# Performance work log

Measured on AMD Instinct MI355X. Metric: run time of the kernel, lower is better.

The kernel has to match this reference:

```python
import jax, jax.numpy as jnp
import numpy as np

B, T, D, H = 8, 2048, 1024, 64

def setup_inputs() -> dict:
    key = jax.random.key(0)
    kx, kq, kk, kv = jax.random.split(key, 4)
    x = jax.random.normal(kx, (B, T, D), dtype=jnp.float32)
    # Linear(embd_size, head_size, bias=False) weights, stored as [D, H] for x @ W
    Wq = jax.random.normal(kq, (D, H), dtype=jnp.float32) * (D ** -0.5)
    Wk = jax.random.normal(kk, (D, H), dtype=jnp.float32) * (D ** -0.5)
    Wv = jax.random.normal(kv, (D, H), dtype=jnp.float32) * (D ** -0.5)
    return {"x": x, "Wq": Wq, "Wk": Wk, "Wv": Wv}

def reference(x, Wq, Wk, Wv):
    Tcur = x.shape[1]
    q = x @ Wq  # [B, T, H]
    k = x @ Wk
    v = x @ Wv
    scores = jnp.einsum('bth,bsh->bts', q, k)
    # NOTE: faithful to source quirk: scores are MULTIPLIED by sqrt(T)
    scores = scores * (Tcur ** 0.5)
    causal = jnp.tril(jnp.ones((Tcur, Tcur), dtype=bool))
    scores = jnp.where(causal, scores, -jnp.inf)
    attn = jax.nn.softmax(scores, axis=2)  # dropout p=0.0 -> identity
    return jnp.einsum('bts,bsh->bth', attn, v)
```

## Files before the change

### kernel.cpp

```cpp
#include <hip/hip_runtime.h>
#include <hip/hip_bf16.h>

#define BB 8
#define TT 2048
#define DD 1024
#define HH 64
#define NROWS (BB*TT)
#define SCALE 45.25483399593904f
#define SPLIT 4

typedef __attribute__((ext_vector_type(8))) short short8;
typedef __attribute__((ext_vector_type(4))) float f32x4;

__device__ inline ushort bf16rne(float f) {
    unsigned u = __float_as_uint(f);
    return (ushort)((u + 0x7fffu + ((u >> 16) & 1u)) >> 16);
}
__device__ inline void bfsplit(float f, ushort& hi, ushort& lo) {
    hi = bf16rne(f);
    float fh = __uint_as_float(((unsigned)hi) << 16);
    lo = bf16rne(f - fh);
}
__device__ inline void split_pack8(const float* v, int4& h4, int4& l4) {
    ushort h[8], l[8];
    #pragma unroll
    for (int j = 0; j < 8; ++j) bfsplit(v[j], h[j], l[j]);
    h4 = make_int4((int)(h[0] | ((unsigned)h[1] << 16)), (int)(h[2] | ((unsigned)h[3] << 16)),
                   (int)(h[4] | ((unsigned)h[5] << 16)), (int)(h[6] | ((unsigned)h[7] << 16)));
    l4 = make_int4((int)(l[0] | ((unsigned)l[1] << 16)), (int)(l[2] | ((unsigned)l[3] << 16)),
                   (int)(l[4] | ((unsigned)l[5] << 16)), (int)(l[6] | ((unsigned)l[7] << 16)));
}

__device__ inline void gload_lds16(const void* g, void* l) {
    __builtin_amdgcn_global_load_lds(
        (const __attribute__((address_space(1))) unsigned int*)(uintptr_t)(g),
        (__attribute__((address_space(3))) unsigned int*)(uintptr_t)(l),
        16, 0, 0);
}

__global__ __launch_bounds__(256) void wprep_kernel(
        const float* __restrict__ Wq, const float* __restrict__ Wk,
        const float* __restrict__ Wv,
        ushort* __restrict__ WpHi, ushort* __restrict__ WpLo) {
    __shared__ float ws[64 * 65];
    const int m = blockIdx.x >> 4;
    const int c = blockIdx.x & 15;
    const float* W = (m == 0) ? Wq : (m == 1) ? Wk : Wv;
    const int tid = threadIdx.x;

    #pragma unroll
    for (int p = 0; p < 4; ++p) {
        int i = tid + p * 256;
        int r = i >> 4, q4 = i & 15;
        float4 v = *(const float4*)(W + (size_t)(c * 64 + r) * 64 + q4 * 4);
        ws[r * 65 + q4 * 4 + 0] = v.x;
        ws[r * 65 + q4 * 4 + 1] = v.y;
        ws[r * 65 + q4 * 4 + 2] = v.z;
        ws[r * 65 + q4 * 4 + 3] = v.w;
    }
    __syncthreads();

    #pragma unroll
    for (int p = 0; p < 2; ++p) {
        int gi = tid + p * 256;
        int nn = gi >> 3, g8 = gi & 7;
        int o  = g8 ^ (nn & 7);
        float v[8];
        #pragma unroll
        for (int j = 0; j < 8; ++j) v[j] = ws[(o * 8 + j) * 65 + nn];
        int4 h4, l4; split_pack8(v, h4, l4);
        size_t base = (size_t)c * 12288 + (size_t)(m * 64 + nn) * 64 + g8 * 8;
        *(int4*)(WpHi + base) = h4;
        *(int4*)(WpLo + base) = l4;
    }
}

__global__ __launch_bounds__(256) void qkv_kernel(
        const float* __restrict__ x,
        const ushort* __restrict__ WpHi, const ushort* __restrict__ WpLo,
        float* __restrict__ Qo, ushort* __restrict__ KhiP,
        ushort* __restrict__ KloP, ushort* __restrict__ VtP) {
    __shared__ ushort Ahi[32 * 64], Alo[32 * 64];
    __shared__ ushort Bhi[192 * 64], Blo[192 * 64];
    const int tid  = threadIdx.x;
    const int lane = tid & 63;
    const int w    = tid >> 6;
    const int n15  = lane & 15;
    const int g    = lane >> 4;
    const int csw  = n15 & 7;
    const int row0 = blockIdx.x * 32;

    f32x4 acc[2][3];
    #pragma unroll
    for (int ms = 0; ms < 2; ++ms)
        #pragma unroll
        for (int nt = 0; nt < 3; ++nt) acc[ms][nt] = (f32x4)0.f;

    const int ar = tid >> 3, aoc = tid & 7;
    const float* xrow = x + (size_t)(row0 + ar) * 1024 + aoc * 8;
    const int adi = ar * 64 + ((aoc ^ (ar & 7)) << 3);

    for (int c = 0; c < 16; ++c) {
        __syncthreads();
        {
            const ushort* sh = WpHi + (size_t)c * 12288 + (size_t)lane * 8;
            const ushort* sl = WpLo + (size_t)c * 12288 + (size_t)lane * 8;
            #pragma unroll
            for (int p = 0; p < 6; ++p) {
                int j = w * 6 + p;
                gload_lds16(sh + j * 512, &Bhi[j * 512]);
                gload_lds16(sl + j * 512, &Blo[j * 512]);
            }
        }
        {
            const float* src = xrow + c * 64;
            float v[8];
            *(float4*)v       = *(const float4*)src;
            *(float4*)(v + 4) = *(const float4*)(src + 4);
            int4 h4, l4; split_pack8(v, h4, l4);
            *(int4*)&Ahi[adi] = h4;
            *(int4*)&Alo[adi] = l4;
        }
        __syncthreads();

        #pragma unroll
        for (int kh = 0; kh < 2; ++kh) {
            short8 afh[2], afl[2], bfh[3], bfl[3];
            #pragma unroll
            for (int ms = 0; ms < 2; ++ms) {
                int ridx = (ms * 16 + n15) * 64 + (((4 * kh + g) ^ csw) << 3);
                afh[ms] = *(const short8*)&Ahi[ridx];
                afl[ms] = *(const short8*)&Alo[ridx];
            }
            #pragma unroll
            for (int nt = 0; nt < 3; ++nt) {
                int nr = w * 48 + nt * 16 + n15;
                int ridx = nr * 64 + (((4 * kh + g) ^ csw) << 3);
                bfh[nt] = *(const short8*)&Bhi[ridx];
                bfl[nt] = *(const short8*)&Blo[ridx];
            }
            #pragma unroll
            for (int nt = 0; nt < 3; ++nt)
                #pragma unroll
                for (int ms = 0; ms < 2; ++ms) {
                    acc[ms][nt] = __builtin_amdgcn_mfma_f32_16x16x32_bf16(
                        afh[ms], bfh[nt], acc[ms][nt], 0, 0, 0);
                    acc[ms][nt] = __builtin_amdgcn_mfma_f32_16x16x32_bf16(
                        afl[ms], bfh[nt], acc[ms][nt], 0, 0, 0);
                    acc[ms][nt] = __builtin_amdgcn_mfma_f32_16x16x32_bf16(
                        afh[ms], bfl[nt], acc[ms][nt], 0, 0, 0);
                }
        }
    }

    const int b  = row0 >> 11;
    const int t0 = row0 & 2047;
    #pragma unroll
    for (int nt = 0; nt < 3; ++nt) {
        const int nglob = w * 48 + nt * 16 + n15;
        const int mat = nglob >> 6;
        const int h = nglob & 63;
        #pragma unroll
        for (int ms = 0; ms < 2; ++ms) {
            const int mb = row0 + ms * 16 + 4 * g;
            if (mat == 0) {
                #pragma unroll
                for (int r = 0; r < 4; ++r)
                    Qo[(size_t)(mb + r) * 64 + h] = acc[ms][nt][r];
            } else if (mat == 1) {
                #pragma unroll
                for (int r = 0; r < 4; ++r) {
                    ushort hi, lo; bfsplit(acc[ms][nt][r], hi, lo);
                    KhiP[(size_t)(mb + r) * 64 + h] = hi;
                    KloP[(size_t)(mb + r) * 64 + h] = lo;
                }
            } else {
                ushort pk[4];
                #pragma unroll
                for (int r = 0; r < 4; ++r) pk[r] = bf16rne(acc[ms][nt][r]);
                const int tloc = t0 + ms * 16 + 4 * g;
                *(uint2*)&VtP[((size_t)(b * 64 + h)) * 2048 + tloc] =
                    make_uint2(pk[0] | ((unsigned)pk[1] << 16),
                               pk[2] | ((unsigned)pk[3] << 16));
            }
        }
    }
}

__global__ __launch_bounds__(128) void attn_kernel(
        const float* __restrict__ Q, const ushort* __restrict__ Khi,
        const ushort* __restrict__ Klo, const ushort* __restrict__ Vt,
        float* __restrict__ Pacc, float* __restrict__ Pm,
        float* __restrict__ Pl) {
    __shared__ ushort KhiL[64 * 64];
    __shared__ ushort KloL[64 * 64];
    __shared__ ushort VtL[64 * 64];
    const int tid  = threadIdx.x;
    const int lane = tid & 63;
    const int w    = tid >> 6;
    const int n    = lane & 15;
    const int g    = lane >> 4;
    const int b    = blockIdx.y;
    const int xx   = blockIdx.x;
    const int qt   = 63 - (xx >> 2);
    const int sp   = xx & 3;
    const int q0   = qt * 32;
    const int qmin = q0 + w * 16;
    const int qrow = qmin + n;
    const int csw  = n & 7;
    const int ntiles = (q0 >> 6) + 1;
    const int it0  = (ntiles * sp) >> 2;
    const int it1  = (ntiles * (sp + 1)) >> 2;

    short8 qhi0, qhi1, qlo0, qlo1;
    {
        const float* qp = Q + ((size_t)b * TT + qrow) * HH + 8 * g;
        float v0[8], v1[8];
        *(float4*)(v0)     = *(const float4*)(qp);
        *(float4*)(v0 + 4) = *(const float4*)(qp + 4);
        *(float4*)(v1)     = *(const float4*)(qp + 32);
        *(float4*)(v1 + 4) = *(const float4*)(qp + 36);
        #pragma unroll
        for (int j = 0; j < 8; ++j) {
            ushort hi, lo;
            bfsplit(v0[j], hi, lo); qhi0[j] = (short)hi; qlo0[j] = (short)lo;
            bfsplit(v1[j], hi, lo); qhi1[j] = (short)hi; qlo1[j] = (short)lo;
        }
    }

    f32x4 accO[4];
    #pragma unroll
    for (int t = 0; t < 4; ++t) accO[t] = (f32x4)0.f;
    float m = -1e30f, l = 0.f;

    const ushort* gkh = Khi + (size_t)b * TT * HH;
    const ushort* gkl = Klo + (size_t)b * TT * HH;
    const ushort* gvt = Vt + (size_t)b * 64 * TT;

    const int crow = lane >> 3;
    const int coct = lane & 7;

    for (int it = it0; it < it1; ++it) {
        const int kb = it * 64;
        __syncthreads();
        #pragma unroll
        for (int p = 0; p < 4; ++p) {
            const int cc  = w * 4 + p;
            const int row = (cc << 3) + crow;
            const int soc = coct ^ (row & 7);
            gload_lds16(gkh + (size_t)(kb + row) * HH + (soc << 3), &KhiL[cc << 9]);
            gload_lds16(gkl + (size_t)(kb + row) * HH + (soc << 3), &KloL[cc << 9]);
            gload_lds16(gvt + (size_t)row * TT + kb + (soc << 3),   &VtL[cc << 9]);
        }
        __syncthreads();

        f32x4 s4[4];
        #pragma unroll
        for (int s = 0; s < 4; ++s) {
            const int keyl = 16 * s + n;
            const ushort* kbase = &KhiL[keyl << 6];
            const ushort* lbase = &KloL[keyl << 6];
            short8 kh0 = *(const short8*)(kbase + ((g ^ csw) << 3));
            short8 kh1 = *(const short8*)(kbase + (((4 + g) ^ csw) << 3));
            short8 kl0 = *(const short8*)(lbase + ((g ^ csw) << 3));
            short8 kl1 = *(const short8*)(lbase + (((4 + g) ^ csw) << 3));
            f32x4 a = (f32x4)0.f;
            a = __builtin_amdgcn_mfma_f32_16x16x32_bf16(kh0, qhi0, a, 0, 0, 0);
            a = __builtin_amdgcn_mfma_f32_16x16x32_bf16(kh1, qhi1, a, 0, 0, 0);
            a = __builtin_amdgcn_mfma_f32_16x16x32_bf16(kl0, qhi0, a, 0, 0, 0);
            a = __builtin_amdgcn_mfma_f32_16x16x32_bf16(kl1, qhi1, a, 0, 0, 0);
            a = __builtin_amdgcn_mfma_f32_16x16x32_bf16(kh0, qlo0, a, 0, 0, 0);
            a = __builtin_amdgcn_mfma_f32_16x16x32_bf16(kh1, qlo1, a, 0, 0, 0);
            s4[s] = a;
        }

        float sm[16];
        if (kb + 63 > qmin) {
            #pragma unroll
            for (int s = 0; s < 4; ++s)
                #pragma unroll
                for (int r = 0; r < 4; ++r) {
                    int keyg = kb + 16 * s + 4 * g + r;
                    sm[s * 4 + r] = (keyg <= qrow) ? s4[s][r] * SCALE : -1e30f;
                }
        } else {
            #pragma unroll
            for (int s = 0; s < 4; ++s)
                #pragma unroll
                for (int r = 0; r < 4; ++r) sm[s * 4 + r] = s4[s][r] * SCALE;
        }
        float pm = sm[0];
        #pragma unroll
        for (int i = 1; i < 16; ++i) pm = fmaxf(pm, sm[i]);
        pm = fmaxf(pm, __shfl_xor(pm, 16));
        pm = fmaxf(pm, __shfl_xor(pm, 32));
        float mn = fmaxf(m, pm);
        float es = __expf(m - mn);
        float p[16], ps = 0.f;
        #pragma unroll
        for (int i = 0; i < 16; ++i) { p[i] = __expf(sm[i] - mn); ps += p[i]; }
        ps += __shfl_xor(ps, 16);
        ps += __shfl_xor(ps, 32);
        l = l * es + ps;
        m = mn;
        #pragma unroll
        for (int t = 0; t < 4; ++t)
            #pragma unroll
            for (int r = 0; r < 4; ++r) accO[t][r] *= es;

        short8 pf0, pf1;
        #pragma unroll
        for (int j = 0; j < 4; ++j) {
            pf0[j]     = (short)bf16rne(p[0 * 4 + j]);
            pf0[j + 4] = (short)bf16rne(p[1 * 4 + j]);
            pf1[j]     = (short)bf16rne(p[2 * 4 + j]);
            pf1[j + 4] = (short)bf16rne(p[3 * 4 + j]);
        }

        #pragma unroll
        for (int t = 0; t < 4; ++t) {
            const int h = 16 * t + n;
            const ushort* vb = &VtL[h << 6];
            union { int2 d[2]; short8 v; } u0, u1;
            u0.d[0] = *(const int2*)(vb + ((4 * g) ^ (csw << 3)));
            u0.d[1] = *(const int2*)(vb + ((16 + 4 * g) ^ (csw << 3)));
            u1.d[0] = *(const int2*)(vb + ((32 + 4 * g) ^ (csw << 3)));
            u1.d[1] = *(const int2*)(vb + ((48 + 4 * g) ^ (csw << 3)));
            accO[t] = __builtin_amdgcn_mfma_f32_16x16x32_bf16(u0.v, pf0, accO[t], 0, 0, 0);
            accO[t] = __builtin_amdgcn_mfma_f32_16x16x32_bf16(u1.v, pf1, accO[t], 0, 0, 0);
        }
    }

    const size_t brow = (size_t)b * TT + qrow;
    float* pa = Pacc + ((size_t)sp * NROWS + brow) * 64 + 4 * g;
    #pragma unroll
    for (int t = 0; t < 4; ++t)
        *(f32x4*)(pa + 16 * t) = accO[t];
    if (g == 0) {
        Pm[(size_t)sp * NROWS + brow] = m;
        Pl[(size_t)sp * NROWS + brow] = l;
    }
}

__global__ __launch_bounds__(256) void combine_kernel(
        const float* __restrict__ Pacc, const float* __restrict__ Pm,
        const float* __restrict__ Pl, float* __restrict__ out) {
    const int u    = blockIdx.x * 256 + threadIdx.x;
    const int row  = u >> 2;
    const int quad = u & 3;

    float ms[SPLIT], ls[SPLIT], M = -1e30f;
    #pragma unroll
    for (int s = 0; s < SPLIT; ++s) {
        ms[s] = Pm[(size_t)s * NROWS + row];
        ls[s] = Pl[(size_t)s * NROWS + row];
        M = fmaxf(M, ms[s]);
    }
    float wgt[SPLIT], den = 0.f;
    #pragma unroll
    for (int s = 0; s < SPLIT; ++s) {
        wgt[s] = __expf(ms[s] - M);
        den += wgt[s] * ls[s];
    }
    const float inv = 1.0f / den;

    float4 o[4];
    #pragma unroll
    for (int i = 0; i < 4; ++i) o[i] = make_float4(0.f, 0.f, 0.f, 0.f);
    #pragma unroll
    for (int s = 0; s < SPLIT; ++s) {
        const float4* a = (const float4*)(Pacc + ((size_t)s * NROWS + row) * 64 + quad * 16);
        #pragma unroll
        for (int i = 0; i < 4; ++i) {
            float4 v = a[i];
            o[i].x += wgt[s] * v.x; o[i].y += wgt[s] * v.y;
            o[i].z += wgt[s] * v.z; o[i].w += wgt[s] * v.w;
        }
    }
    float4* op = (float4*)(out + (size_t)row * 64 + quad * 16);
    #pragma unroll
    for (int i = 0; i < 4; ++i)
        op[i] = make_float4(o[i].x * inv, o[i].y * inv, o[i].z * inv, o[i].w * inv);
}

extern "C" void kernel_launch(void* const* d_in, const int* in_sizes, int n_in,
                              void* d_out, int out_size, void* d_ws, size_t ws_size,
                              hipStream_t stream) {
    const float* x  = (const float*)d_in[0];
    const float* Wq = (const float*)d_in[1];
    const float* Wk = (const float*)d_in[2];
    const float* Wv = (const float*)d_in[3];
    float* outp = (float*)d_out;

    float*  Qw   = (float*)d_ws;
    ushort* KhiP = (ushort*)(Qw + (size_t)NROWS * HH);
    ushort* KloP = KhiP + (size_t)NROWS * HH;
    ushort* VtP  = KloP + (size_t)NROWS * HH;
    ushort* WpHi = VtP + (size_t)NROWS * HH;
    ushort* WpLo = WpHi + (size_t)3 * 64 * 1024;
    float*  Pacc = (float*)(WpLo + (size_t)3 * 64 * 1024);
    float*  Pm   = Pacc + (size_t)SPLIT * NROWS * HH;
    float*  Pl   = Pm + (size_t)SPLIT * NROWS;

    wprep_kernel<<<48, 256, 0, stream>>>(Wq, Wk, Wv, WpHi, WpLo);
    qkv_kernel<<<NROWS / 32, 256, 0, stream>>>(x, WpHi, WpLo, Qw, KhiP, KloP, VtP);
    attn_kernel<<<dim3(64 * SPLIT, BB), 128, 0, stream>>>(Qw, KhiP, KloP, VtP,
                                                          Pacc, Pm, Pl);
    combine_kernel<<<NROWS * 4 / 256, 256, 0, stream>>>(Pacc, Pm, Pl, outp);
}
```

Before: 71.84 us.

## Double-buffer QKV weight tiles, split output columns across grid, per-wave A tiles

```diff
diff --git a/kernel.cpp b/kernel.cpp
--- a/kernel.cpp
+++ b/kernel.cpp
@@ -80,109 +80,129 @@
         const ushort* __restrict__ WpHi, const ushort* __restrict__ WpLo,
         float* __restrict__ Qo, ushort* __restrict__ KhiP,
         ushort* __restrict__ KloP, ushort* __restrict__ VtP) {
-    __shared__ ushort Ahi[32 * 64], Alo[32 * 64];
-    __shared__ ushort Bhi[192 * 64], Blo[192 * 64];
+    __shared__ ushort Bhi[2][96 * 64];
+    __shared__ ushort Blo[2][96 * 64];
+    __shared__ ushort Aws[4][2048];
     const int tid  = threadIdx.x;
     const int lane = tid & 63;
     const int w    = tid >> 6;
+    const int wr   = w >> 1;
+    const int wc   = w & 1;
     const int n15  = lane & 15;
     const int g    = lane >> 4;
     const int csw  = n15 & 7;
     const int row0 = blockIdx.x * 32;
-
-    f32x4 acc[2][3];
-    #pragma unroll
-    for (int ms = 0; ms < 2; ++ms)
-        #pragma unroll
-        for (int nt = 0; nt < 3; ++nt) acc[ms][nt] = (f32x4)0.f;
-
-    const int ar = tid >> 3, aoc = tid & 7;
-    const float* xrow = x + (size_t)(row0 + ar) * 1024 + aoc * 8;
-    const int adi = ar * 64 + ((aoc ^ (ar & 7)) << 3);
-
+    const int nh   = blockIdx.y;
+
+    ushort* myA = Aws[w];
+
+    f32x4 acc[3];
+    #pragma unroll
+    for (int nt = 0; nt < 3; ++nt) acc[nt] = (f32x4)0.f;
+
+    const int arow = wr * 16 + (lane >> 2);
+    const int o0   = (lane & 3) << 1;
+    const float* xp = x + (size_t)(row0 + arow) * 1024 + o0 * 8;
+    const int r7 = arow & 7;
+    const int adst0 = (arow & 15) * 64 + ((o0 ^ r7) << 3);
+    const int adst1 = (arow & 15) * 64 + (((o0 + 1) ^ r7) << 3);
+
+    const ushort* wsh = WpHi + (size_t)nh * 6144 + (size_t)lane * 8;
+    const ushort* wsl = WpLo + (size_t)nh * 6144 + (size_t)lane * 8;
+
+    float xv[16];
+    *(float4*)(xv)      = *(const float4*)(xp);
+    *(float4*)(xv + 4)  = *(const float4*)(xp + 4);
+    *(float4*)(xv + 8)  = *(const float4*)(xp + 8);
+    *(float4*)(xv + 12) = *(const float4*)(xp + 12);
+    #pragma unroll
+    for (int p = 0; p < 3; ++p) {
+        int j = w * 3 + p;
+        gload_lds16(wsh + j * 512, &Bhi[0][j * 512]);
+        gload_lds16(wsl + j * 512, &Blo[0][j * 512]);
+    }
+    __syncthreads();
+
+    int cur = 0;
     for (int c = 0; c < 16; ++c) {
+        if (c + 1 < 16) {
+            const ushort* sh = wsh + (size_t)(c + 1) * 12288;
+            const ushort* sl = wsl + (size_t)(c + 1) * 12288;
+            #pragma unroll
+            for (int p = 0; p < 3; ++p) {
+                int j = w * 3 + p;
+                gload_lds16(sh + j * 512, &Bhi[cur ^ 1][j * 512]);
+                gload_lds16(sl + j * 512, &Blo[cur ^ 1][j * 512]);
+            }
+        }
+        {
+            int4 h4, l4;
+            split_pack8(xv, h4, l4);
+            *(int4*)&myA[adst0]        = h4;
+            *(int4*)&myA[1024 + adst0] = l4;
+            split_pack8(xv + 8, h4, l4);
+            *(int4*)&myA[adst1]        = h4;
+            *(int4*)&myA[1024 + adst1] = l4;
+        }
+        if (c + 1 < 16) {
+            const float* src = xp + (c + 1) * 64;
+            *(float4*)(xv)      = *(const float4*)(src);
+            *(float4*)(xv + 4)  = *(const float4*)(src + 4);
+            *(float4*)(xv + 8)  = *(const float4*)(src + 8);
+            *(float4*)(xv + 12) = *(const float4*)(src + 12);
+        }
+        const ushort* bh = Bhi[cur];
+        const ushort* bl = Blo[cur];
+        #pragma unroll
+        for (int kh = 0; kh < 2; ++kh) {
+            const int o = 4 * kh + g;
+            short8 afh = *(const short8*)&myA[n15 * 64 + ((o ^ csw) << 3)];
+            short8 afl = *(const short8*)&myA[1024 + n15 * 64 + ((o ^ csw) << 3)];
+            short8 bfh[3], bfl[3];
+            #pragma unroll
+            for (int nt = 0; nt < 3; ++nt) {
+                int ridx = (wc * 48 + nt * 16 + n15) * 64 + ((o ^ csw) << 3);
+                bfh[nt] = *(const short8*)&bh[ridx];
+                bfl[nt] = *(const short8*)&bl[ridx];
+            }
+            #pragma unroll
+            for (int nt = 0; nt < 3; ++nt) {
+                acc[nt] = __builtin_amdgcn_mfma_f32_16x16x32_bf16(afh, bfh[nt], acc[nt], 0, 0, 0);
+                acc[nt] = __builtin_amdgcn_mfma_f32_16x16x32_bf16(afl, bfh[nt], acc[nt], 0, 0, 0);
+                acc[nt] = __builtin_amdgcn_mfma_f32_16x16x32_bf16(afh, bfl[nt], acc[nt], 0, 0, 0);
+            }
+        }
         __syncthreads();
-        {
-            const ushort* sh = WpHi + (size_t)c * 12288 + (size_t)lane * 8;
-            const ushort* sl = WpLo + (size_t)c * 12288 + (size_t)lane * 8;
-            #pragma unroll
-            for (int p = 0; p < 6; ++p) {
-                int j = w * 6 + p;
-                gload_lds16(sh + j * 512, &Bhi[j * 512]);
-                gload_lds16(sl + j * 512, &Blo[j * 512]);
-            }
-        }
-        {
-            const float* src = xrow + c * 64;
-            float v[8];
-            *(float4*)v       = *(const float4*)src;
-            *(float4*)(v + 4) = *(const float4*)(src + 4);
-            int4 h4, l4; split_pack8(v, h4, l4);
-            *(int4*)&Ahi[adi] = h4;
-            *(int4*)&Alo[adi] = l4;
-        }
-        __syncthreads();
-
-        #pragma unroll
-        for (int kh = 0; kh < 2; ++kh) {
-            short8 afh[2], afl[2], bfh[3], bfl[3];
-            #pragma unroll
-            for (int ms = 0; ms < 2; ++ms) {
-                int ridx = (ms * 16 + n15) * 64 + (((4 * kh + g) ^ csw) << 3);
-                afh[ms] = *(const short8*)&Ahi[ridx];
-                afl[ms] = *(const short8*)&Alo[ridx];
-            }
-            #pragma unroll
-            for (int nt = 0; nt < 3; ++nt) {
-                int nr = w * 48 + nt * 16 + n15;
-                int ridx = nr * 64 + (((4 * kh + g) ^ csw) << 3);
-                bfh[nt] = *(const short8*)&Bhi[ridx];
-                bfl[nt] = *(const short8*)&Blo[ridx];
-            }
-            #pragma unroll
-            for (int nt = 0; nt < 3; ++nt)
-                #pragma unroll
-                for (int ms = 0; ms < 2; ++ms) {
-                    acc[ms][nt] = __builtin_amdgcn_mfma_f32_16x16x32_bf16(
-                        afh[ms], bfh[nt], acc[ms][nt], 0, 0, 0);
-                    acc[ms][nt] = __builtin_amdgcn_mfma_f32_16x16x32_bf16(
-                        afl[ms], bfh[nt], acc[ms][nt], 0, 0, 0);
-                    acc[ms][nt] = __builtin_amdgcn_mfma_f32_16x16x32_bf16(
-                        afh[ms], bfl[nt], acc[ms][nt], 0, 0, 0);
-                }
-        }
+        cur ^= 1;
     }
 
     const int b  = row0 >> 11;
     const int t0 = row0 & 2047;
+    const int mb = row0 + wr * 16 + 4 * g;
     #pragma unroll
     for (int nt = 0; nt < 3; ++nt) {
-        const int nglob = w * 48 + nt * 16 + n15;
-        const int mat = nglob >> 6;
-        const int h = nglob & 63;
-        #pragma unroll
-        for (int ms = 0; ms < 2; ++ms) {
-            const int mb = row0 + ms * 16 + 4 * g;
-            if (mat == 0) {
-                #pragma unroll
-                for (int r = 0; r < 4; ++r)
-                    Qo[(size_t)(mb + r) * 64 + h] = acc[ms][nt][r];
-            } else if (mat == 1) {
-                #pragma unroll
-                for (int r = 0; r < 4; ++r) {
-                    ushort hi, lo; bfsplit(acc[ms][nt][r], hi, lo);
-                    KhiP[(size_t)(mb + r) * 64 + h] = hi;
-                    KloP[(size_t)(mb + r) * 64 + h] = lo;
-                }
-            } else {
-                ushort pk[4];
-                #pragma unroll
-                for (int r = 0; r < 4; ++r) pk[r] = bf16rne(acc[ms][nt][r]);
-                const int tloc = t0 + ms * 16 + 4 * g;
-                *(uint2*)&VtP[((size_t)(b * 64 + h)) * 2048 + tloc] =
-                    make_uint2(pk[0] | ((unsigned)pk[1] << 16),
-                               pk[2] | ((unsigned)pk[3] << 16));
+        const int col = nh * 96 + wc * 48 + nt * 16 + n15;
+        const int mat = col >> 6;
+        const int h   = col & 63;
+        if (mat == 0) {
+            #pragma unroll
+            for (int r = 0; r < 4; ++r)
+                Qo[(size_t)(mb + r) * 64 + h] = acc[nt][r];
+        } else if (mat == 1) {
+            #pragma unroll
+            for (int r = 0; r < 4; ++r) {
+                ushort hi, lo; bfsplit(acc[nt][r], hi, lo);
+                KhiP[(size_t)(mb + r) * 64 + h] = hi;
+                KloP[(size_t)(mb + r) * 64 + h] = lo;
             }
+        } else {
+            ushort pk[4];
+            #pragma unroll
+            for (int r = 0; r < 4; ++r) pk[r] = bf16rne(acc[nt][r]);
+            const int tloc = t0 + wr * 16 + 4 * g;
+            *(uint2*)&VtP[((size_t)(b * 64 + h)) * 2048 + tloc] =
+                make_uint2(pk[0] | ((unsigned)pk[1] << 16),
+                           pk[2] | ((unsigned)pk[3] << 16));
         }
     }
 }
@@ -403,7 +423,7 @@
     float*  Pl   = Pm + (size_t)SPLIT * NROWS;
 
     wprep_kernel<<<48, 256, 0, stream>>>(Wq, Wk, Wv, WpHi, WpLo);
-    qkv_kernel<<<NROWS / 32, 256, 0, stream>>>(x, WpHi, WpLo, Qw, KhiP, KloP, VtP);
+    qkv_kernel<<<dim3(NROWS / 32, 2), 256, 0, stream>>>(x, WpHi, WpLo, Qw, KhiP, KloP, VtP);
     attn_kernel<<<dim3(64 * SPLIT, BB), 128, 0, stream>>>(Qw, KhiP, KloP, VtP,
                                                           Pacc, Pm, Pl);
     combine_kernel<<<NROWS * 4 / 256, 256, 0, stream>>>(Pacc, Pm, Pl, outp);
```

After: 92.06 us. 1.28x slower.

## Double-buffer QKV projection LDS tiles and prefetch x several chunks ahead

Applied to the files above, without the earlier changes.

```diff
diff --git a/kernel.cpp b/kernel.cpp
--- a/kernel.cpp
+++ b/kernel.cpp
@@ -8,6 +8,7 @@
 #define NROWS (BB*TT)
 #define SCALE 45.25483399593904f
 #define SPLIT 4
+#define NC 32
 
 typedef __attribute__((ext_vector_type(8))) short short8;
 typedef __attribute__((ext_vector_type(4))) float f32x4;
@@ -29,6 +30,13 @@
                    (int)(h[4] | ((unsigned)h[5] << 16)), (int)(h[6] | ((unsigned)h[7] << 16)));
     l4 = make_int4((int)(l[0] | ((unsigned)l[1] << 16)), (int)(l[2] | ((unsigned)l[3] << 16)),
                    (int)(l[4] | ((unsigned)l[5] << 16)), (int)(l[6] | ((unsigned)l[7] << 16)));
+}
+__device__ inline void split_pack4(float4 v, uint2& h, uint2& l) {
+    ushort h0, h1, h2, h3, l0, l1, l2, l3;
+    bfsplit(v.x, h0, l0); bfsplit(v.y, h1, l1);
+    bfsplit(v.z, h2, l2); bfsplit(v.w, h3, l3);
+    h = make_uint2(h0 | ((unsigned)h1 << 16), h2 | ((unsigned)h3 << 16));
+    l = make_uint2(l0 | ((unsigned)l1 << 16), l2 | ((unsigned)l3 << 16));
 }
 
 __device__ inline void gload_lds16(const void* g, void* l) {
@@ -44,7 +52,7 @@
         ushort* __restrict__ WpHi, ushort* __restrict__ WpLo) {
     __shared__ float ws[64 * 65];
     const int m = blockIdx.x >> 4;
-    const int c = blockIdx.x & 15;
+    const int c16 = blockIdx.x & 15;
     const float* W = (m == 0) ? Wq : (m == 1) ? Wk : Wv;
     const int tid = threadIdx.x;
 
@@ -52,7 +60,7 @@
     for (int p = 0; p < 4; ++p) {
         int i = tid + p * 256;
         int r = i >> 4, q4 = i & 15;
-        float4 v = *(const float4*)(W + (size_t)(c * 64 + r) * 64 + q4 * 4);
+        float4 v = *(const float4*)(W + (size_t)(c16 * 64 + r) * 64 + q4 * 4);
         ws[r * 65 + q4 * 4 + 0] = v.x;
         ws[r * 65 + q4 * 4 + 1] = v.y;
         ws[r * 65 + q4 * 4 + 2] = v.z;
@@ -64,30 +72,33 @@
     for (int p = 0; p < 2; ++p) {
         int gi = tid + p * 256;
         int nn = gi >> 3, g8 = gi & 7;
-        int o  = g8 ^ (nn & 7);
         float v[8];
         #pragma unroll
-        for (int j = 0; j < 8; ++j) v[j] = ws[(o * 8 + j) * 65 + nn];
+        for (int j = 0; j < 8; ++j) v[j] = ws[(g8 * 8 + j) * 65 + nn];
         int4 h4, l4; split_pack8(v, h4, l4);
-        size_t base = (size_t)c * 12288 + (size_t)(m * 64 + nn) * 64 + g8 * 8;
+        const int c32 = c16 * 2 + (g8 >> 2);
+        const int o   = g8 & 3;
+        const int col = m * 64 + nn;
+        const int op  = o ^ (col & 3);
+        size_t base = (size_t)c32 * 6144 + (size_t)col * 32 + (op << 3);
         *(int4*)(WpHi + base) = h4;
         *(int4*)(WpLo + base) = l4;
     }
 }
 
-__global__ __launch_bounds__(256) void qkv_kernel(
+__global__ __launch_bounds__(256, 2) void qkv_kernel(
         const float* __restrict__ x,
         const ushort* __restrict__ WpHi, const ushort* __restrict__ WpLo,
         float* __restrict__ Qo, ushort* __restrict__ KhiP,
         ushort* __restrict__ KloP, ushort* __restrict__ VtP) {
-    __shared__ ushort Ahi[32 * 64], Alo[32 * 64];
-    __shared__ ushort Bhi[192 * 64], Blo[192 * 64];
+    __shared__ ushort Ahi[2][32 * 32], Alo[2][32 * 32];
+    __shared__ ushort Bhi[2][192 * 32], Blo[2][192 * 32];
     const int tid  = threadIdx.x;
     const int lane = tid & 63;
     const int w    = tid >> 6;
     const int n15  = lane & 15;
     const int g    = lane >> 4;
-    const int csw  = n15 & 7;
+    const int cx   = n15 & 3;
     const int row0 = blockIdx.x * 32;
 
     f32x4 acc[2][3];
@@ -96,61 +107,76 @@
         #pragma unroll
         for (int nt = 0; nt < 3; ++nt) acc[ms][nt] = (f32x4)0.f;
 
-    const int ar = tid >> 3, aoc = tid & 7;
-    const float* xrow = x + (size_t)(row0 + ar) * 1024 + aoc * 8;
-    const int adi = ar * 64 + ((aoc ^ (ar & 7)) << 3);
-
-    for (int c = 0; c < 16; ++c) {
-        __syncthreads();
+    const int xr = tid >> 3, xq = tid & 7;
+    const float* xp = x + (size_t)(row0 + xr) * 1024 + xq * 4;
+    const int aoct = xq >> 1;
+    const int adst = xr * 32 + ((aoct ^ (xr & 3)) << 3) + ((xq & 1) << 2);
+
+    const ushort* wsh = WpHi + (size_t)lane * 8;
+    const ushort* wsl = WpLo + (size_t)lane * 8;
+
+    float4 x0 = *(const float4*)(xp);
+    float4 xA = *(const float4*)(xp + 32);
+    float4 xB = *(const float4*)(xp + 64);
+    #pragma unroll
+    for (int p = 0; p < 3; ++p) {
+        int j = w * 3 + p;
+        gload_lds16(wsh + j * 512, &Bhi[0][j * 512]);
+        gload_lds16(wsl + j * 512, &Blo[0][j * 512]);
+    }
+    {
+        uint2 h, l; split_pack4(x0, h, l);
+        *(uint2*)&Ahi[0][adst] = h;
+        *(uint2*)&Alo[0][adst] = l;
+    }
+    __syncthreads();
+
+    int cur = 0;
+    for (int c = 0; c < NC; ++c) {
+        const int c3 = (c + 3 < NC) ? c + 3 : NC - 1;
+        float4 xN = *(const float4*)(xp + c3 * 32);
+        const int c1 = (c + 1 < NC) ? c + 1 : NC - 1;
         {
-            const ushort* sh = WpHi + (size_t)c * 12288 + (size_t)lane * 8;
-            const ushort* sl = WpLo + (size_t)c * 12288 + (size_t)lane * 8;
+            const ushort* sh = wsh + (size_t)c1 * 6144;
+            const ushort* sl = wsl + (size_t)c1 * 6144;
             #pragma unroll
-            for (int p = 0; p < 6; ++p) {
-                int j = w * 6 + p;
-                gload_lds16(sh + j * 512, &Bhi[j * 512]);
-                gload_lds16(sl + j * 512, &Blo[j * 512]);
+            for (int p = 0; p < 3; ++p) {
+                int j = w * 3 + p;
+                gload_lds16(sh + j * 512, &Bhi[cur ^ 1][j * 512]);
+                gload_lds16(sl + j * 512, &Blo[cur ^ 1][j * 512]);
             }
         }
         {
-            const float* src = xrow + c * 64;
-            float v[8];
-            *(float4*)v       = *(const float4*)src;
-            *(float4*)(v + 4) = *(const float4*)(src + 4);
-            int4 h4, l4; split_pack8(v, h4, l4);
-            *(int4*)&Ahi[adi] = h4;
-            *(int4*)&Alo[adi] = l4;
-        }
-        __syncthreads();
-
-        #pragma unroll
-        for (int kh = 0; kh < 2; ++kh) {
-            short8 afh[2], afl[2], bfh[3], bfl[3];
+            uint2 h, l; split_pack4(xA, h, l);
+            *(uint2*)&Ahi[cur ^ 1][adst] = h;
+            *(uint2*)&Alo[cur ^ 1][adst] = l;
+        }
+        short8 afh[2], afl[2], bfh[3], bfl[3];
+        #pragma unroll
+        for (int ms = 0; ms < 2; ++ms) {
+            int ao = (ms * 16 + n15) * 32 + ((g ^ cx) << 3);
+            afh[ms] = *(const short8*)&Ahi[cur][ao];
+            afl[ms] = *(const short8*)&Alo[cur][ao];
+        }
+        #pragma unroll
+        for (int nt = 0; nt < 3; ++nt) {
+            int bo = (w * 48 + nt * 16 + n15) * 32 + ((g ^ cx) << 3);
+            bfh[nt] = *(const short8*)&Bhi[cur][bo];
+            bfl[nt] = *(const short8*)&Blo[cur][bo];
+        }
+        #pragma unroll
+        for (int nt = 0; nt < 3; ++nt)
             #pragma unroll
             for (int ms = 0; ms < 2; ++ms) {
-                int ridx = (ms * 16 + n15) * 64 + (((4 * kh + g) ^ csw) << 3);
-                afh[ms] = *(const short8*)&Ahi[ridx];
-                afl[ms] = *(const short8*)&Alo[ridx];
+                acc[ms][nt] = __builtin_amdgcn_mfma_f32_16x16x32_bf16(
+                    afh[ms], bfh[nt], acc[ms][nt], 0, 0, 0);
+                acc[ms][nt] = __builtin_amdgcn_mfma_f32_16x16x32_bf16(
+                    afl[ms], bfh[nt], acc[ms][nt], 0, 0, 0);
+                acc[ms][nt] = __builtin_amdgcn_mfma_f32_16x16x32_bf16(
+                    afh[ms], bfl[nt], acc[ms][nt], 0, 0, 0);
             }
-            #pragma unroll
-            for (int nt = 0; nt < 3; ++nt) {
-                int nr = w * 48 + nt * 16 + n15;
-                int ridx = nr * 64 + (((4 * kh + g) ^ csw) << 3);
-                bfh[nt] = *(const short8*)&Bhi[ridx];
-                bfl[nt] = *(const short8*)&Blo[ridx];
-            }
-            #pragma unroll
-            for (int nt = 0; nt < 3; ++nt)
-                #pragma unroll
-                for (int ms = 0; ms < 2; ++ms) {
-                    acc[ms][nt] = __builtin_amdgcn_mfma_f32_16x16x32_bf16(
-                        afh[ms], bfh[nt], acc[ms][nt], 0, 0, 0);
-                    acc[ms][nt] = __builtin_amdgcn_mfma_f32_16x16x32_bf16(
-                        afl[ms], bfh[nt], acc[ms][nt], 0, 0, 0);
-                    acc[ms][nt] = __builtin_amdgcn_mfma_f32_16x16x32_bf16(
-                        afh[ms], bfl[nt], acc[ms][nt], 0, 0, 0);
-                }
-        }
+        __syncthreads();
+        xA = xB; xB = xN; cur ^= 1;
     }
 
     const int b  = row0 >> 11;
```

New measurement: 80.55 us. 12.1% more time.

## Double-buffer QKV projection LDS tiles and double the row tile per block

Applied to the files above, without the earlier changes.

```diff
diff --git a/kernel.cpp b/kernel.cpp
--- a/kernel.cpp
+++ b/kernel.cpp
@@ -75,20 +75,22 @@
     }
 }
 
-__global__ __launch_bounds__(256) void qkv_kernel(
+__global__ __launch_bounds__(512) void qkv_kernel(
         const float* __restrict__ x,
         const ushort* __restrict__ WpHi, const ushort* __restrict__ WpLo,
         float* __restrict__ Qo, ushort* __restrict__ KhiP,
         ushort* __restrict__ KloP, ushort* __restrict__ VtP) {
-    __shared__ ushort Ahi[32 * 64], Alo[32 * 64];
-    __shared__ ushort Bhi[192 * 64], Blo[192 * 64];
+    __shared__ ushort Ahi[2][64 * 64], Alo[2][64 * 64];
+    __shared__ ushort Bhi[2][192 * 64], Blo[2][192 * 64];
     const int tid  = threadIdx.x;
     const int lane = tid & 63;
     const int w    = tid >> 6;
+    const int wm   = w >> 2;
+    const int wn   = w & 3;
     const int n15  = lane & 15;
     const int g    = lane >> 4;
     const int csw  = n15 & 7;
-    const int row0 = blockIdx.x * 32;
+    const int row0 = blockIdx.x * 64;
 
     f32x4 acc[2][3];
     #pragma unroll
@@ -100,44 +102,66 @@
     const float* xrow = x + (size_t)(row0 + ar) * 1024 + aoc * 8;
     const int adi = ar * 64 + ((aoc ^ (ar & 7)) << 3);
 
+    const ushort* wsh = WpHi + (size_t)lane * 8;
+    const ushort* wsl = WpLo + (size_t)lane * 8;
+
+    {
+        float v[8];
+        *(float4*)v       = *(const float4*)(xrow);
+        *(float4*)(v + 4) = *(const float4*)(xrow + 4);
+        int4 h4, l4; split_pack8(v, h4, l4);
+        *(int4*)&Ahi[0][adi] = h4;
+        *(int4*)&Alo[0][adi] = l4;
+    }
+    #pragma unroll
+    for (int p = 0; p < 3; ++p) {
+        int j = w * 3 + p;
+        gload_lds16(wsh + j * 512, &Bhi[0][j * 512]);
+        gload_lds16(wsl + j * 512, &Blo[0][j * 512]);
+    }
+    float xA[8], xB[8];
+    *(float4*)(xA)     = *(const float4*)(xrow + 64);
+    *(float4*)(xA + 4) = *(const float4*)(xrow + 68);
+    *(float4*)(xB)     = *(const float4*)(xrow + 128);
+    *(float4*)(xB + 4) = *(const float4*)(xrow + 132);
+    __syncthreads();
+
+    int cur = 0;
     for (int c = 0; c < 16; ++c) {
-        __syncthreads();
+        const int c3 = (c + 3 < 16) ? c + 3 : 15;
+        float xN[8];
+        *(float4*)(xN)     = *(const float4*)(xrow + c3 * 64);
+        *(float4*)(xN + 4) = *(const float4*)(xrow + c3 * 64 + 4);
+        const int c1 = (c + 1 < 16) ? c + 1 : 15;
         {
-            const ushort* sh = WpHi + (size_t)c * 12288 + (size_t)lane * 8;
-            const ushort* sl = WpLo + (size_t)c * 12288 + (size_t)lane * 8;
-            #pragma unroll
-            for (int p = 0; p < 6; ++p) {
-                int j = w * 6 + p;
-                gload_lds16(sh + j * 512, &Bhi[j * 512]);
-                gload_lds16(sl + j * 512, &Blo[j * 512]);
+            const ushort* sh = wsh + (size_t)c1 * 12288;
+            const ushort* sl = wsl + (size_t)c1 * 12288;
+            #pragma unroll
+            for (int p = 0; p < 3; ++p) {
+                int j = w * 3 + p;
+                gload_lds16(sh + j * 512, &Bhi[cur ^ 1][j * 512]);
+                gload_lds16(sl + j * 512, &Blo[cur ^ 1][j * 512]);
             }
         }
         {
-            const float* src = xrow + c * 64;
-            float v[8];
-            *(float4*)v       = *(const float4*)src;
-            *(float4*)(v + 4) = *(const float4*)(src + 4);
-            int4 h4, l4; split_pack8(v, h4, l4);
-            *(int4*)&Ahi[adi] = h4;
-            *(int4*)&Alo[adi] = l4;
-        }
-        __syncthreads();
-
+            int4 h4, l4; split_pack8(xA, h4, l4);
+            *(int4*)&Ahi[cur ^ 1][adi] = h4;
+            *(int4*)&Alo[cur ^ 1][adi] = l4;
+        }
         #pragma unroll
         for (int kh = 0; kh < 2; ++kh) {
             short8 afh[2], afl[2], bfh[3], bfl[3];
             #pragma unroll
             for (int ms = 0; ms < 2; ++ms) {
-                int ridx = (ms * 16 + n15) * 64 + (((4 * kh + g) ^ csw) << 3);
-                afh[ms] = *(const short8*)&Ahi[ridx];
-                afl[ms] = *(const short8*)&Alo[ridx];
+                int ao = (wm * 32 + ms * 16 + n15) * 64 + (((4 * kh + g) ^ csw) << 3);
+                afh[ms] = *(const short8*)&Ahi[cur][ao];
+                afl[ms] = *(const short8*)&Alo[cur][ao];
             }
             #pragma unroll
             for (int nt = 0; nt < 3; ++nt) {
-                int nr = w * 48 + nt * 16 + n15;
-                int ridx = nr * 64 + (((4 * kh + g) ^ csw) << 3);
-                bfh[nt] = *(const short8*)&Bhi[ridx];
-                bfl[nt] = *(const short8*)&Blo[ridx];
+                int bo = (wn * 48 + nt * 16 + n15) * 64 + (((4 * kh + g) ^ csw) << 3);
+                bfh[nt] = *(const short8*)&Bhi[cur][bo];
+                bfl[nt] = *(const short8*)&Blo[cur][bo];
             }
             #pragma unroll
             for (int nt = 0; nt < 3; ++nt)
@@ -151,18 +175,22 @@
                         afh[ms], bfl[nt], acc[ms][nt], 0, 0, 0);
                 }
         }
+        __syncthreads();
+        #pragma unroll
+        for (int j = 0; j < 8; ++j) { xA[j] = xB[j]; xB[j] = xN[j]; }
+        cur ^= 1;
     }
 
     const int b  = row0 >> 11;
     const int t0 = row0 & 2047;
     #pragma unroll
     for (int nt = 0; nt < 3; ++nt) {
-        const int nglob = w * 48 + nt * 16 + n15;
-        const int mat = nglob >> 6;
-        const int h = nglob & 63;
+        const int col = wn * 48 + nt * 16 + n15;
+        const int mat = col >> 6;
+        const int h   = col & 63;
         #pragma unroll
         for (int ms = 0; ms < 2; ++ms) {
-            const int mb = row0 + ms * 16 + 4 * g;
+            const int mb = row0 + wm * 32 + ms * 16 + 4 * g;
             if (mat == 0) {
                 #pragma unroll
                 for (int r = 0; r < 4; ++r)
@@ -178,7 +206,7 @@
                 ushort pk[4];
                 #pragma unroll
                 for (int r = 0; r < 4; ++r) pk[r] = bf16rne(acc[ms][nt][r]);
-                const int tloc = t0 + ms * 16 + 4 * g;
+                const int tloc = t0 + wm * 32 + ms * 16 + 4 * g;
                 *(uint2*)&VtP[((size_t)(b * 64 + h)) * 2048 + tloc] =
                     make_uint2(pk[0] | ((unsigned)pk[1] << 16),
                                pk[2] | ((unsigned)pk[3] << 16));
@@ -403,7 +431,7 @@
     float*  Pl   = Pm + (size_t)SPLIT * NROWS;
 
     wprep_kernel<<<48, 256, 0, stream>>>(Wq, Wk, Wv, WpHi, WpLo);
-    qkv_kernel<<<NROWS / 32, 256, 0, stream>>>(x, WpHi, WpLo, Qw, KhiP, KloP, VtP);
+    qkv_kernel<<<NROWS / 64, 512, 0, stream>>>(x, WpHi, WpLo, Qw, KhiP, KloP, VtP);
     attn_kernel<<<dim3(64 * SPLIT, BB), 128, 0, stream>>>(Qw, KhiP, KloP, VtP,
                                                           Pacc, Pm, Pl);
     combine_kernel<<<NROWS * 4 / 256, 256, 0, stream>>>(Pacc, Pm, Pl, outp);
```

New measurement: 72.03 us. Within noise of the previous version (+0.3%).
